# Kernel optimization log

Measured on AMD Instinct MI355X. Metric: run time of the kernel, lower is better.

Reference implementation:

```python
import jax, jax.numpy as jnp
import numpy as np

TEMPERATURE = 1.0
EPS = 1e-8
B, D, N, K = 2048, 32, 8192, 30


def setup_inputs() -> dict:
    key = jax.random.key(0)
    k1, k2, k3 = jax.random.split(key, 3)
    z_current = jax.random.normal(k1, (B, D), dtype=jnp.float32)
    pre_knn_indices = jax.random.randint(k2, (N, K), 0, N, dtype=jnp.int64 if jax.config.jax_enable_x64 else jnp.int32)
    sample_indices = jax.random.randint(k3, (B,), 0, N, dtype=jnp.int64 if jax.config.jax_enable_x64 else jnp.int32)
    return {"z_current": z_current, "pre_knn_indices": pre_knn_indices, "sample_indices": sample_indices}


def reference(z_current, pre_knn_indices, sample_indices):
    b = z_current.shape[0]
    eye = jnp.eye(b, dtype=bool)
    # pairwise Euclidean distance via gram trick: (B,B), avoids (B,B,D) intermediate
    sq = jnp.sum(z_current * z_current, axis=-1)
    d2 = jnp.maximum(sq[:, None] + sq[None, :] - 2.0 * (z_current @ z_current.T), 0.0)
    d2_safe = jnp.where(eye, 1.0, d2)  # avoid sqrt(0) on diagonal (masked below anyway)
    dist = jnp.sqrt(d2_safe)
    sim = jnp.where(eye, -jnp.inf, -dist / TEMPERATURE)
    soft_neighbors = jax.nn.softmax(sim, axis=1)  # (B,B)
    # neighbor mask: j is kept iff global id of j is in pre-kNN set of i, and j != i
    knn = pre_knn_indices[sample_indices]  # (B,K) global ids of i's pre-neighbors
    in_set = (knn[:, :, None] == sample_indices[None, None, :]).any(axis=1)  # (B,B)
    mask = in_set & ~eye
    s = jnp.sum(soft_neighbors * mask, axis=1)  # (B,)
    valid = mask.any(axis=1)
    count = valid.sum()
    loss_i = -jnp.log(s + EPS)
    total = jnp.sum(jnp.where(valid, loss_i, 0.0))
    return jnp.where(count > 0, total / count, jnp.float32(0.0))
```

## Files before the change

kernel.cpp:

```cpp
#include <hip/hip_runtime.h>
#include <math.h>

#define Bsz 2048
#define Ddim 32
#define Nsz 8192
#define Kk 30
#define TPB 256
#define ROWS 4
#define JCH (Bsz / TPB)
#define NBLK (Bsz / ROWS)
#define NW (Nsz / 32)

__global__ __launch_bounds__(TPB, 2) void softnp_main(
    const float* __restrict__ z,
    const int*   __restrict__ pre_knn,
    const int*   __restrict__ samp,
    float*       __restrict__ wsloss,
    float*       __restrict__ wscnt)
{
    __shared__ unsigned bits4[NW][ROWS];
    __shared__ float    zish[ROWS * Ddim];
    __shared__ int      rowsi[ROWS];
    __shared__ float    rden[4][ROWS], rnum[4][ROWS];

    const int t  = threadIdx.x;
    const int i0 = blockIdx.x * ROWS;

    #pragma unroll
    for (int c = 0; c < (NW * ROWS) / TPB; ++c)
        ((unsigned*)bits4)[t + c * TPB] = 0u;
    if (t < ROWS * Ddim) zish[t] = z[(size_t)i0 * Ddim + t];
    if (t < ROWS) rowsi[t] = samp[i0 + t];
    __syncthreads();

    if (t < ROWS * 32) {
        const int r = t >> 5, k = t & 31;
        if (k < Kk) {
            const int id = pre_knn[(size_t)rowsi[r] * Kk + k];
            atomicOr(&bits4[id >> 5][r], 1u << (id & 31));
        }
    }

    float4 zi[ROWS][Ddim / 4];
    const float4* z4s = (const float4*)zish;
    #pragma unroll
    for (int r = 0; r < ROWS; ++r)
        #pragma unroll
        for (int d = 0; d < Ddim / 4; ++d)
            zi[r][d] = z4s[r * (Ddim / 4) + d];

    float si2[ROWS];
    #pragma unroll
    for (int r = 0; r < ROWS; ++r) {
        float s = 0.f;
        #pragma unroll
        for (int d = 0; d < Ddim / 4; ++d)
            s += zi[r][d].x * zi[r][d].x + zi[r][d].y * zi[r][d].y
               + zi[r][d].z * zi[r][d].z + zi[r][d].w * zi[r][d].w;
        si2[r] = s;
    }
    __syncthreads();

    float den[ROWS] = {0.f, 0.f, 0.f, 0.f};
    float num[ROWS] = {0.f, 0.f, 0.f, 0.f};

    const float4* zg = (const float4*)z;
    int j = t;
    float4 cur[8];
    #pragma unroll
    for (int d = 0; d < 8; ++d) cur[d] = zg[(size_t)j * 8 + d];
    int scur = samp[j];

    #pragma unroll
    for (int c = 0; c < JCH; ++c) {
        float4 nxt[8];
        int snxt = 0;
        if (c + 1 < JCH) {
            #pragma unroll
            for (int d = 0; d < 8; ++d) nxt[d] = zg[(size_t)(j + TPB) * 8 + d];
            snxt = samp[j + TPB];
        }

        float dot[ROWS] = {0.f, 0.f, 0.f, 0.f};
        float sj2 = 0.f;
        #pragma unroll
        for (int d = 0; d < 8; ++d) {
            const float4 v = cur[d];
            sj2 += v.x * v.x + v.y * v.y + v.z * v.z + v.w * v.w;
            #pragma unroll
            for (int r = 0; r < ROWS; ++r)
                dot[r] += zi[r][d].x * v.x + zi[r][d].y * v.y
                        + zi[r][d].z * v.z + zi[r][d].w * v.w;
        }

        const int   sj = scur;
        const uint4 bw = ((const uint4*)bits4)[sj >> 5];
        const unsigned bsel[4] = {bw.x, bw.y, bw.z, bw.w};
        #pragma unroll
        for (int r = 0; r < ROWS; ++r) {
            const float d2 = fmaxf(si2[r] + sj2 - 2.f * dot[r], 0.f);
            const bool diag = (j == i0 + r);
            const float e = diag ? 0.f : __expf(-sqrtf(d2));
            den[r] += e;
            if (!diag && ((bsel[r] >> (sj & 31)) & 1u)) num[r] += e;
        }

        if (c + 1 < JCH) {
            #pragma unroll
            for (int d = 0; d < 8; ++d) cur[d] = nxt[d];
            scur = snxt;
        }
        j += TPB;
    }

    const int lane = t & 63, wv = t >> 6;
    #pragma unroll
    for (int r = 0; r < ROWS; ++r) {
        #pragma unroll
        for (int off = 32; off > 0; off >>= 1) {
            den[r] += __shfl_xor(den[r], off, 64);
            num[r] += __shfl_xor(num[r], off, 64);
        }
    }
    if (lane == 0) {
        #pragma unroll
        for (int r = 0; r < ROWS; ++r) { rden[wv][r] = den[r]; rnum[wv][r] = num[r]; }
    }
    __syncthreads();

    if (t < ROWS) {
        float D = 0.f, Nm = 0.f;
        #pragma unroll
        for (int w = 0; w < 4; ++w) { D += rden[w][t]; Nm += rnum[w][t]; }
        float lr = 0.f, vr = 0.f;
        if (Nm > 0.f) {
            lr = -__logf(Nm / D + 1e-8f);
            vr = 1.f;
        }
        lr += __shfl_xor(lr, 1, 64); vr += __shfl_xor(vr, 1, 64);
        lr += __shfl_xor(lr, 2, 64); vr += __shfl_xor(vr, 2, 64);
        if (t == 0) { wsloss[blockIdx.x] = lr; wscnt[blockIdx.x] = vr; }
    }
}

__global__ __launch_bounds__(TPB) void softnp_final(
    const float* __restrict__ wsloss,
    const float* __restrict__ wscnt,
    float*       __restrict__ out)
{
    __shared__ float rl[4], rc[4];
    const int t = threadIdx.x;
    float L = wsloss[t] + wsloss[t + TPB];
    float C = wscnt[t] + wscnt[t + TPB];
    #pragma unroll
    for (int off = 32; off > 0; off >>= 1) {
        L += __shfl_xor(L, off, 64);
        C += __shfl_xor(C, off, 64);
    }
    const int lane = t & 63, wv = t >> 6;
    if (lane == 0) { rl[wv] = L; rc[wv] = C; }
    __syncthreads();
    if (t == 0) {
        const float Ls = rl[0] + rl[1] + rl[2] + rl[3];
        const float Cs = rc[0] + rc[1] + rc[2] + rc[3];
        out[0] = (Cs > 0.f) ? Ls / Cs : 0.f;
    }
}

extern "C" void kernel_launch(void* const* d_in, const int* in_sizes, int n_in,
                              void* d_out, int out_size, void* d_ws, size_t ws_size,
                              hipStream_t stream)
{
    const float* z       = (const float*)d_in[0];
    const int*   pre_knn = (const int*)d_in[1];
    const int*   samp    = (const int*)d_in[2];
    float*       out     = (float*)d_out;
    float*       wsloss  = (float*)d_ws;
    float*       wscnt   = wsloss + NBLK;

    softnp_main<<<dim3(NBLK), dim3(TPB), 0, stream>>>(z, pre_knn, samp, wsloss, wscnt);
    softnp_final<<<dim3(1), dim3(TPB), 0, stream>>>(wsloss, wscnt, out);
}
```

Before: 77.02 us.

## Halve rows per block, raise occupancy, drop manual register prefetch

```diff
diff --git a/kernel.cpp b/kernel.cpp
--- a/kernel.cpp
+++ b/kernel.cpp
@@ -6,19 +6,19 @@
 #define Nsz 8192
 #define Kk 30
 #define TPB 256
-#define ROWS 4
+#define ROWS 2
 #define JCH (Bsz / TPB)
 #define NBLK (Bsz / ROWS)
 #define NW (Nsz / 32)
 
-__global__ __launch_bounds__(TPB, 2) void softnp_main(
+__global__ __launch_bounds__(TPB, 4) void softnp_main(
     const float* __restrict__ z,
     const int*   __restrict__ pre_knn,
     const int*   __restrict__ samp,
     float*       __restrict__ wsloss,
     float*       __restrict__ wscnt)
 {
-    __shared__ unsigned bits4[NW][ROWS];
+    __shared__ unsigned bits2[NW][ROWS];
     __shared__ float    zish[ROWS * Ddim];
     __shared__ int      rowsi[ROWS];
     __shared__ float    rden[4][ROWS], rnum[4][ROWS];
@@ -26,9 +26,8 @@
     const int t  = threadIdx.x;
     const int i0 = blockIdx.x * ROWS;
 
-    #pragma unroll
-    for (int c = 0; c < (NW * ROWS) / TPB; ++c)
-        ((unsigned*)bits4)[t + c * TPB] = 0u;
+    ((unsigned*)bits2)[t]       = 0u;
+    ((unsigned*)bits2)[t + TPB] = 0u;
     if (t < ROWS * Ddim) zish[t] = z[(size_t)i0 * Ddim + t];
     if (t < ROWS) rowsi[t] = samp[i0 + t];
     __syncthreads();
@@ -37,7 +36,7 @@
         const int r = t >> 5, k = t & 31;
         if (k < Kk) {
             const int id = pre_knn[(size_t)rowsi[r] * Kk + k];
-            atomicOr(&bits4[id >> 5][r], 1u << (id & 31));
+            atomicOr(&bits2[id >> 5][r], 1u << (id & 31));
         }
     }
 
@@ -61,41 +60,32 @@
     }
     __syncthreads();
 
-    float den[ROWS] = {0.f, 0.f, 0.f, 0.f};
-    float num[ROWS] = {0.f, 0.f, 0.f, 0.f};
+    float den[ROWS] = {0.f, 0.f};
+    float num[ROWS] = {0.f, 0.f};
 
     const float4* zg = (const float4*)z;
     int j = t;
-    float4 cur[8];
-    #pragma unroll
-    for (int d = 0; d < 8; ++d) cur[d] = zg[(size_t)j * 8 + d];
-    int scur = samp[j];
-
     #pragma unroll
     for (int c = 0; c < JCH; ++c) {
-        float4 nxt[8];
-        int snxt = 0;
-        if (c + 1 < JCH) {
-            #pragma unroll
-            for (int d = 0; d < 8; ++d) nxt[d] = zg[(size_t)(j + TPB) * 8 + d];
-            snxt = samp[j + TPB];
-        }
+        float4 v[8];
+        #pragma unroll
+        for (int d = 0; d < 8; ++d) v[d] = zg[(size_t)j * 8 + d];
+        const int sj = samp[j];
 
-        float dot[ROWS] = {0.f, 0.f, 0.f, 0.f};
+        float dot[ROWS] = {0.f, 0.f};
         float sj2 = 0.f;
         #pragma unroll
         for (int d = 0; d < 8; ++d) {
-            const float4 v = cur[d];
-            sj2 += v.x * v.x + v.y * v.y + v.z * v.z + v.w * v.w;
+            const float4 u = v[d];
+            sj2 += u.x * u.x + u.y * u.y + u.z * u.z + u.w * u.w;
             #pragma unroll
             for (int r = 0; r < ROWS; ++r)
-                dot[r] += zi[r][d].x * v.x + zi[r][d].y * v.y
-                        + zi[r][d].z * v.z + zi[r][d].w * v.w;
+                dot[r] += zi[r][d].x * u.x + zi[r][d].y * u.y
+                        + zi[r][d].z * u.z + zi[r][d].w * u.w;
         }
 
-        const int   sj = scur;
-        const uint4 bw = ((const uint4*)bits4)[sj >> 5];
-        const unsigned bsel[4] = {bw.x, bw.y, bw.z, bw.w};
+        const uint2 bw = ((const uint2*)bits2)[sj >> 5];
+        const unsigned bsel[ROWS] = {bw.x, bw.y};
         #pragma unroll
         for (int r = 0; r < ROWS; ++r) {
             const float d2 = fmaxf(si2[r] + sj2 - 2.f * dot[r], 0.f);
@@ -103,12 +93,6 @@
             const float e = diag ? 0.f : __expf(-sqrtf(d2));
             den[r] += e;
             if (!diag && ((bsel[r] >> (sj & 31)) & 1u)) num[r] += e;
-        }
-
-        if (c + 1 < JCH) {
-            #pragma unroll
-            for (int d = 0; d < 8; ++d) cur[d] = nxt[d];
-            scur = snxt;
         }
         j += TPB;
     }
@@ -138,7 +122,6 @@
             vr = 1.f;
         }
         lr += __shfl_xor(lr, 1, 64); vr += __shfl_xor(vr, 1, 64);
-        lr += __shfl_xor(lr, 2, 64); vr += __shfl_xor(vr, 2, 64);
         if (t == 0) { wsloss[blockIdx.x] = lr; wscnt[blockIdx.x] = vr; }
     }
 }
@@ -150,8 +133,12 @@
 {
     __shared__ float rl[4], rc[4];
     const int t = threadIdx.x;
-    float L = wsloss[t] + wsloss[t + TPB];
-    float C = wscnt[t] + wscnt[t + TPB];
+    float L = 0.f, C = 0.f;
+    #pragma unroll
+    for (int c = 0; c < NBLK / TPB; ++c) {
+        L += wsloss[t + c * TPB];
+        C += wscnt[t + c * TPB];
+    }
     #pragma unroll
     for (int off = 32; off > 0; off >>= 1) {
         L += __shfl_xor(L, off, 64);
```

Measured after the change: 90.50 us. 17.5% more time.
